# Optimization experiments

Measured on AMD Instinct MI355X. Metric: run time of the kernel, lower is better.

## Reference

```python
import jax, jax.numpy as jnp
import numpy as np
from jax import lax

WINS = [3, 5, 7, 11, 15, 19]
MAXW = 19
PAD = MAXW // 2 + 1          # 10, matches F.pad(..., max_wh//2+1)
NEG_HALF = (-MAXW) // 2      # -10, matches torch's `-self.max_wh // 2` (floor div)
EPS_IN = 1e-5
EPS_DEV = 1e-6


def _conv(x, w, b, dil):
    # x: [B,C,H,W], w: [O,I,kh,kw], 'same' padding with dilation
    y = lax.conv_general_dilated(x, w, (1, 1), 'SAME',
                                 rhs_dilation=(dil, dil),
                                 dimension_numbers=('NCHW', 'OIHW', 'NCHW'))
    return y + b[None, :, None, None]


def _inorm_relu(y):
    # InstanceNorm2d(affine=False): per-sample per-channel over H,W, biased var
    m = jnp.mean(y, axis=(2, 3), keepdims=True)
    v = jnp.mean((y - m) ** 2, axis=(2, 3), keepdims=True)
    return jax.nn.relu((y - m) * lax.rsqrt(v + EPS_IN))


def _integral(x):
    # x: [B,H,W,C] -> padded double cumsum (integral image) [B,H+2P,W+2P,C]
    xp = jnp.pad(x, ((0, 0), (PAD, PAD), (PAD, PAD), (0, 0)))
    return jnp.cumsum(jnp.cumsum(xp, axis=1), axis=2)


def _box_sum(ii, h, w):
    # 4-corner integral-image lookup; slices reproduce torch offsets exactly
    top = MAXW // 2 - h // 2
    bot = top + h
    left = MAXW // 2 - w // 2
    right = left + w
    top0 = NEG_HALF - h // 2 - 1
    bot0 = top0 + h
    left0 = NEG_HALF - w // 2 - 1
    right0 = left0 + w
    return (ii[:, top:top0, left:left0] + ii[:, bot:bot0, right:right0]
            - ii[:, top:top0, right:right0] - ii[:, bot:bot0, left:left0])


def _multi_window_mean(x):
    # x: [B,H,W,1] -> [B,n_wins,H,W,1] of window means
    ii = _integral(x)
    cnt_ii = _integral(jnp.ones_like(x[:1]))  # [1,...] pixel-count integral
    means = [_box_sum(ii, hw, hw) / _box_sum(cnt_ii, hw, hw) for hw in WINS]
    return jnp.stack(means, axis=1)


def _sauvola(x1, k, R):
    E_x = _multi_window_mean(x1)
    E_x2 = _multi_window_mean(x1 * x1)
    dev = jnp.sqrt(jnp.maximum(E_x2 - E_x ** 2, EPS_DEV))
    return E_x * (1.0 + k * (dev / R - 1.0))  # [B,n,H,W,1]


def setup_inputs() -> dict:
    key = jax.random.key(0)
    ks = jax.random.split(key, 16)
    B, H, W = 4, 768, 768
    base = 4
    chans = [1, 4, 8, 12, 16, 20, 24]
    d = {'x': jax.random.uniform(ks[0], (B, 1, H, W), dtype=jnp.float32)}
    names = ['conv1', 'convs1', 'convs2', 'convs3', 'convs4', 'convs5']
    for i, nm in enumerate(names):
        cin, cout = chans[i], chans[i + 1]
        d[nm + '_w'] = jax.random.normal(ks[1 + i], (cout, cin, 3, 3), dtype=jnp.float32) * 0.1
        d[nm + '_b'] = jax.random.normal(ks[7 + i], (cout,), dtype=jnp.float32) * 0.01
    d['conv2_w'] = jax.random.normal(ks[13], (len(WINS), 24, 3, 3), dtype=jnp.float32) * 0.1
    d['conv2_b'] = jax.random.normal(ks[14], (len(WINS),), dtype=jnp.float32) * 0.01
    d['k'] = jnp.full((1, len(WINS), 1, 1, 1), 0.2, dtype=jnp.float32)
    d['R'] = jnp.full((1, len(WINS), 1, 1, 1), 0.5, dtype=jnp.float32)
    d['alpha'] = jnp.full((1, 1, 1, 1), 16.0, dtype=jnp.float32)
    return d


def reference(x, conv1_w, conv1_b, convs1_w, convs1_b, convs2_w, convs2_b,
              convs3_w, convs3_b, convs4_w, convs4_b, convs5_w, convs5_b,
              conv2_w, conv2_b, k, R, alpha):
    y = _inorm_relu(_conv(x, conv1_w, conv1_b, 1))
    for w, b in ((convs1_w, convs1_b), (convs2_w, convs2_b), (convs3_w, convs3_b),
                 (convs4_w, convs4_b), (convs5_w, convs5_b)):
        y = _inorm_relu(_conv(y, w, b, 2))
    f = jax.nn.softmax(_conv(y, conv2_w, conv2_b, 1), axis=1)  # [B,n,H,W]
    x1 = jnp.transpose(x, (0, 2, 3, 1))                        # [B,H,W,1]
    th = _sauvola(x1, k, R)                                    # [B,n,H,W,1]
    th1 = jnp.sum(f[..., None] * th, axis=1)                   # [B,H,W,1]
    diff = (x1 - th1) * alpha / (1.0 - 0.0)                    # img_range (0,1)
    return jnp.transpose(diff, (0, 3, 1, 2))                   # [B,1,H,W]
```

## Files before the change

kernel.cpp:

```cpp
#include <hip/hip_runtime.h>
#include <math.h>

#define BDIM 256
#define BDIM2 512
typedef __bf16 bf16;
typedef __bf16 bf16x4 __attribute__((ext_vector_type(4)));
typedef __bf16 bf16x8 __attribute__((ext_vector_type(8)));
typedef float f32x4 __attribute__((ext_vector_type(4)));
typedef float f32x2 __attribute__((ext_vector_type(2)));

template <bool V> struct BC { static constexpr bool value = V; };

constexpr int B_ = 4, H_ = 768, W_ = 768;
constexpr int HW_ = H_ * W_;
constexpr int TS = 16;
constexpr int NTB = W_ / TS;
constexpr int NBLK = HW_ / (TS * TS);
constexpr int TSR = 16, TSC = 32;
constexpr int NTBC = W_ / TSC;
constexpr int NBLKH = (H_ / TSR) * NTBC;

constexpr int PMAX_FLOATS = 4 * NBLK * 48;
constexpr int OUT_ELEMS   = B_ * HW_;

__device__ void repack_one(const float* __restrict__ src, bf16* __restrict__ dst,
                           int CIN, int CINP, int COUT, int NT16, int KPP)
{
    const int n_ = NT16 * KPP;
    for (int idx = threadIdx.x; idx < n_; idx += BDIM) {
        const int n = idx / KPP, k = idx - n * KPP;
        const int tap = k / CINP, ci = k - tap * CINP;
        float v = 0.f;
        if (n < COUT && tap < 9 && ci < CIN)
            v = src[(n * CIN + ci) * 9 + tap];
        dst[idx] = (bf16)v;
    }
}

__global__ __launch_bounds__(BDIM) void repack_all(
    const float* w0, const float* w1, const float* w2, const float* w3,
    const float* w4, const float* w5, const float* wf,
    bf16* r0, bf16* r1, bf16* r2, bf16* r3, bf16* r4, bf16* r5, bf16* rf)
{
    switch (blockIdx.x) {
        case 0: repack_one(w0, r0, 1,  8,  4,  16, 104); break;
        case 1: repack_one(w1, r1, 4,  8,  8,  16, 104); break;
        case 2: repack_one(w2, r2, 8,  8,  12, 16, 104); break;
        case 3: repack_one(w3, r3, 12, 16, 16, 16, 168); break;
        case 4: repack_one(w4, r4, 16, 16, 20, 32, 168); break;
        case 5: repack_one(w5, r5, 20, 24, 24, 32, 232); break;
        case 6: repack_one(wf, rf, 24, 24, 6,  16, 232); break;
    }
}

template <int CIN, int CINP, int COUT, int DIL, bool FIRST>
__global__ __launch_bounds__(BDIM) void conv_mfma(
    const void* __restrict__ inv,
    const float* __restrict__ prevStats,
    const bf16* __restrict__ wp,
    const float* __restrict__ bias,
    bf16* __restrict__ y,
    float* __restrict__ partials,
    int NBT)
{
    constexpr int TW = TS + 2 * DIL;
    constexpr int KP = ((9 * CINP + 31) / 32) * 32;
    constexpr int KPP = KP + 8;
    constexpr int NT = (COUT + 15) / 16;
    constexpr int KS = KP / 32;
    constexpr int CSTR = (CINP == 16) ? 24 : CINP;
    __shared__ __align__(16) bf16 tile[TW * TW * CSTR];
    __shared__ float sred[4][2 * COUT];

    const int s = blockIdx.x / NBLK;
    const int blk = blockIdx.x - s * NBLK;
    const int ti = blk / NTB, tj = blk - ti * NTB;
    const int i0 = ti * TS - DIL, j0 = tj * TS - DIL;
    const int t = threadIdx.x;
    const bool interior = (i0 >= 0) & (j0 >= 0) &
                          (i0 + TW <= H_) & (j0 + TW <= W_);

    const float* ps = prevStats + s * 2 * CIN;
    auto stage = [&](auto bc) {
        constexpr bool IN = decltype(bc)::value;
        for (int loc = t; loc < TW * TW; loc += BDIM) {
            const int rr = loc / TW, cc = loc - rr * TW;
            const int gi = i0 + rr, gj = j0 + cc;
            bool ok = true;
            if constexpr (!IN)
                ok = (gi >= 0) & (gi < H_) & (gj >= 0) & (gj < W_);
            float lv[CSTR];
#pragma unroll
            for (int c = 0; c < CSTR; ++c) lv[c] = 0.f;
            if (ok) {
                if constexpr (FIRST) {
                    const float* xg = (const float*)inv + (size_t)s * HW_;
                    lv[0] = xg[(size_t)gi * W_ + gj];
                } else {
                    const bf16* ing = (const bf16*)inv +
                                      ((size_t)s * HW_ + (size_t)gi * W_ + gj) * CIN;
                    if constexpr (CIN % 8 == 0) {
#pragma unroll
                        for (int qq = 0; qq < CIN / 8; ++qq) {
                            bf16x8 raw = ((const bf16x8*)ing)[qq];
#pragma unroll
                            for (int u = 0; u < 8; ++u) {
                                const int ci = 8 * qq + u;
                                lv[ci] = fmaxf(fmaf((float)raw[u], ps[2 * ci], ps[2 * ci + 1]), 0.f);
                            }
                        }
                    } else {
#pragma unroll
                        for (int qq = 0; qq < CIN / 4; ++qq) {
                            bf16x4 raw = ((const bf16x4*)ing)[qq];
#pragma unroll
                            for (int u = 0; u < 4; ++u) {
                                const int ci = 4 * qq + u;
                                lv[ci] = fmaxf(fmaf((float)raw[u], ps[2 * ci], ps[2 * ci + 1]), 0.f);
                            }
                        }
                    }
                }
            }
            bf16* lp = tile + loc * CSTR;
#pragma unroll
            for (int g = 0; g < CSTR / 8; ++g) {
                bf16x8 pk;
#pragma unroll
                for (int u = 0; u < 8; ++u) pk[u] = (bf16)lv[8 * g + u];
                *(bf16x8*)(lp + 8 * g) = pk;
            }
        }
    };
    if (interior) stage(BC<true>{}); else stage(BC<false>{});
    __syncthreads();

    const int wave = t >> 6, lane = t & 63, q = lane >> 4, ln = lane & 15;
    f32x4 acc[4][NT];
#pragma unroll
    for (int mt = 0; mt < 4; ++mt)
#pragma unroll
        for (int u = 0; u < NT; ++u) acc[mt][u] = (f32x4){0.f, 0.f, 0.f, 0.f};

    auto aOff = [&](int ks) -> int {
        int k0 = ks * 32 + q * 8;
        int tap = k0 / CINP;
        int ci0 = k0 - tap * CINP;
        if (tap > 8) { tap = 0; ci0 = 0; }
        const int ky = tap / 3, kx = tap - 3 * ky;
        return (ky * DIL * TW + kx * DIL) * CSTR + ci0;
    };

    bf16x8 bfr[NT], bfrN[NT];
    bf16x8 af[4], afN[4];
#pragma unroll
    for (int u = 0; u < NT; ++u)
        bfr[u] = *(const bf16x8*)&wp[(u * 16 + ln) * KPP + q * 8];
    {
        const int ao = aOff(0);
#pragma unroll
        for (int mt = 0; mt < 4; ++mt)
            af[mt] = *(const bf16x8*)&tile[((wave * 4 + mt) * TW + ln) * CSTR + ao];
    }

#pragma unroll
    for (int ks = 0; ks < KS; ++ks) {
        if (ks + 1 < KS) {
#pragma unroll
            for (int u = 0; u < NT; ++u)
                bfrN[u] = *(const bf16x8*)&wp[(u * 16 + ln) * KPP + (ks + 1) * 32 + q * 8];
            const int ao = aOff(ks + 1);
#pragma unroll
            for (int mt = 0; mt < 4; ++mt)
                afN[mt] = *(const bf16x8*)&tile[((wave * 4 + mt) * TW + ln) * CSTR + ao];
        }
#pragma unroll
        for (int mt = 0; mt < 4; ++mt)
#pragma unroll
            for (int u = 0; u < NT; ++u)
                acc[mt][u] = __builtin_amdgcn_mfma_f32_16x16x32_bf16(
                    af[mt], bfr[u], acc[mt][u], 0, 0, 0);
#pragma unroll
        for (int u = 0; u < NT; ++u) bfr[u] = bfrN[u];
#pragma unroll
        for (int mt = 0; mt < 4; ++mt) af[mt] = afN[mt];
    }

#pragma unroll
    for (int u = 0; u < NT; ++u) {
        const int n = u * 16 + ln;
        const float bv = (n < COUT) ? bias[n] : 0.f;
        float s1 = 0.f, s2 = 0.f;
#pragma unroll
        for (int mt = 0; mt < 4; ++mt)
#pragma unroll
            for (int r = 0; r < 4; ++r) {
                const float v = acc[mt][u][r] + bv;
                acc[mt][u][r] = v;
                s1 += v; s2 += v * v;
            }
        s1 += __shfl_xor(s1, 16); s1 += __shfl_xor(s1, 32);
        s2 += __shfl_xor(s2, 16); s2 += __shfl_xor(s2, 32);
        if (lane < 16 && n < COUT) { sred[wave][n] = s1; sred[wave][COUT + n] = s2; }
    }
    __syncthreads();
    if (t < 2 * COUT) {
        partials[(size_t)t * NBT + (size_t)s * NBLK + blk] =
            sred[0][t] + sred[1][t] + sred[2][t] + sred[3][t];
    }

    bf16* ost = tile;
#pragma unroll
    for (int u = 0; u < NT; ++u) {
        const int n = u * 16 + ln;
        if (n < COUT) {
#pragma unroll
            for (int mt = 0; mt < 4; ++mt)
#pragma unroll
                for (int r = 0; r < 4; ++r) {
                    const int pl = (wave * 4 + mt) * 16 + q * 4 + r;
                    ost[pl * COUT + n] = (bf16)acc[mt][u][r];
                }
        }
    }
    __syncthreads();

    const int lr = t >> 4, lc = t & 15;
    bf16* yp = y + (size_t)s * HW_ * COUT +
               ((size_t)(ti * TS + lr) * W_ + (tj * TS + lc)) * COUT;
    const bf16* sp = ost + t * COUT;
    if constexpr (COUT % 8 == 0) {
#pragma unroll
        for (int g = 0; g < COUT / 8; ++g)
            ((bf16x8*)yp)[g] = ((const bf16x8*)sp)[g];
    } else {
#pragma unroll
        for (int g = 0; g < COUT / 4; ++g)
            ((bf16x4*)yp)[g] = ((const bf16x4*)sp)[g];
    }
}

template <int COUT>
__global__ __launch_bounds__(BDIM) void reduce_stats(
    const float* __restrict__ partials, float* __restrict__ stats, int NBT)
{
    const int s = blockIdx.x / COUT;
    const int co = blockIdx.x - s * COUT;
    const float* P1 = partials + (size_t)co * NBT + (size_t)s * NBLK;
    const float* P2 = partials + (size_t)(COUT + co) * NBT + (size_t)s * NBLK;
    float s1 = 0.f, s2 = 0.f;
    for (int k = threadIdx.x; k < NBLK; k += BDIM) {
        s1 += P1[k];
        s2 += P2[k];
    }
#pragma unroll
    for (int off = 32; off; off >>= 1) {
        s1 += __shfl_xor(s1, off);
        s2 += __shfl_xor(s2, off);
    }
    __shared__ float l1[4], l2[4];
    const int lane = threadIdx.x & 63, wave = threadIdx.x >> 6;
    if (lane == 0) { l1[wave] = s1; l2[wave] = s2; }
    __syncthreads();
    if (threadIdx.x == 0) {
        float t1 = l1[0] + l1[1] + l1[2] + l1[3];
        float t2 = l2[0] + l2[1] + l2[2] + l2[3];
        float m = t1 / (float)HW_;
        float var = t2 / (float)HW_ - m * m;
        const float rs = rsqrtf(var + 1e-5f);
        stats[((size_t)s * COUT + co) * 2 + 0] = rs;
        stats[((size_t)s * COUT + co) * 2 + 1] = -m * rs;
    }
}

__global__ __launch_bounds__(BDIM2) void conv2_sauvola(
    const bf16* __restrict__ in, const float* __restrict__ prevStats,
    const bf16* __restrict__ wp, const float* __restrict__ bias,
    const float* __restrict__ x,
    const float* __restrict__ kArr, const float* __restrict__ RArr,
    const float* __restrict__ alphaP, float* __restrict__ outp)
{
    constexpr int CIN = 24, CINP = 24, COUT = 6;
    constexpr int TWR = TSR + 2;
    constexpr int TWC = TSC + 2;
    constexpr int KPP = 232, KS = 7, CSTR = 24;
    constexpr int R9 = 9;
    constexpr int HR = TSR + 2 * R9;
    constexpr int HC = TSC + 2 * R9;
    constexpr int IST = 51;
    constexpr int SLOG_STR = 7;
    __shared__ __align__(16) bf16 tile[TWR * TWC * CSTR];
    __shared__ __align__(16) f32x2 I12[(HR + 1) * IST];

    const int s = blockIdx.x / NBLKH;
    const int blk = blockIdx.x - s * NBLKH;
    const int ti = blk / NTBC, tj = blk - ti * NTBC;
    const int i0 = ti * TSR - 1, j0 = tj * TSC - 1;
    const int is0 = ti * TSR - R9, js0 = tj * TSC - R9;
    const int t = threadIdx.x;
    const float* xs = x + (size_t)s * HW_;
    const bool interior = (is0 >= 0) & (js0 >= 0) &
                          (is0 + HR <= H_) & (js0 + HC <= W_);

    const float* ps = prevStats + s * 2 * CIN;
    auto stage = [&](auto bc) {
        constexpr bool IN = decltype(bc)::value;
        for (int loc = t; loc < TWR * TWC; loc += BDIM2) {
            const int rr = loc / TWC, cc = loc - rr * TWC;
            const int gi = i0 + rr, gj = j0 + cc;
            bool ok = true;
            if constexpr (!IN)
                ok = (gi >= 0) & (gi < H_) & (gj >= 0) & (gj < W_);
            float lv[CSTR];
#pragma unroll
            for (int c = 0; c < CSTR; ++c) lv[c] = 0.f;
            if (ok) {
                const bf16* ing = in + ((size_t)s * HW_ + (size_t)gi * W_ + gj) * CIN;
#pragma unroll
                for (int qq = 0; qq < CIN / 8; ++qq) {
                    bf16x8 raw = ((const bf16x8*)ing)[qq];
#pragma unroll
                    for (int u = 0; u < 8; ++u) {
                        const int ci = 8 * qq + u;
                        lv[ci] = fmaxf(fmaf((float)raw[u], ps[2 * ci], ps[2 * ci + 1]), 0.f);
                    }
                }
            }
            bf16* lp = tile + loc * CSTR;
#pragma unroll
            for (int g = 0; g < CSTR / 8; ++g) {
                bf16x8 pk;
#pragma unroll
                for (int u = 0; u < 8; ++u) pk[u] = (bf16)lv[8 * g + u];
                *(bf16x8*)(lp + 8 * g) = pk;
            }
        }
        for (int loc = t; loc < HR * HC; loc += BDIM2) {
            const int rr = loc / HC, cc = loc - rr * HC;
            const int gi = is0 + rr, gj = js0 + cc;
            float v;
            if constexpr (IN) {
                v = xs[(size_t)gi * W_ + gj];
            } else {
                v = 0.f;
                if ((gi >= 0) & (gi < H_) & (gj >= 0) & (gj < W_))
                    v = xs[(size_t)gi * W_ + gj];
            }
            I12[(rr + 1) * IST + cc + 1] = (f32x2){v, v * v};
        }
    };
    if (interior) stage(BC<true>{}); else stage(BC<false>{});
    for (int idx = t; idx < IST + HR; idx += BDIM2) {
        if (idx < IST) I12[idx] = (f32x2){0.f, 0.f};
        else I12[(idx - IST + 1) * IST] = (f32x2){0.f, 0.f};
    }
    __syncthreads();

    const int wave = t >> 6, lane = t & 63, q = lane >> 4, ln = lane & 15;
    f32x4 acc[4];
#pragma unroll
    for (int mt = 0; mt < 4; ++mt) acc[mt] = (f32x4){0.f, 0.f, 0.f, 0.f};

    auto aOff = [&](int ks) -> int {
        int k0 = ks * 32 + q * 8;
        int tap = k0 / CINP;
        int ci0 = k0 - tap * CINP;
        if (tap > 8) { tap = 0; ci0 = 0; }
        const int ky = tap / 3, kx = tap - 3 * ky;
        return (ky * TWC + kx) * CSTR + ci0;
    };

#pragma unroll
    for (int ks = 0; ks < KS; ++ks) {
        const bf16x8 bfr = *(const bf16x8*)&wp[ln * KPP + ks * 32 + q * 8];
        const int ao = aOff(ks);
#pragma unroll
        for (int mt = 0; mt < 4; ++mt) {
            const int Mt = wave * 4 + mt;
            const bf16x8 af = *(const bf16x8*)
                &tile[(((Mt >> 1)) * TWC + (Mt & 1) * 16 + ln) * CSTR + ao];
            acc[mt] = __builtin_amdgcn_mfma_f32_16x16x32_bf16(af, bfr, acc[mt], 0, 0, 0);
        }
    }
    __syncthreads();

    float* slog = (float*)tile;
    const float bv = (ln < COUT) ? bias[ln] : 0.f;
#pragma unroll
    for (int mt = 0; mt < 4; ++mt)
#pragma unroll
        for (int r = 0; r < 4; ++r)
            if (ln < COUT) {
                const int pl = (wave * 4 + mt) * 16 + q * 4 + r;
                slog[pl * SLOG_STR + ln] = acc[mt][r] + bv;
            }
    if (t < HR) {
        f32x2* row = I12 + (t + 1) * IST;
        f32x2 a = (f32x2){0.f, 0.f};
#pragma unroll 2
        for (int c = 1; c <= HC; ++c) { a += row[c]; row[c] = a; }
    }
    __syncthreads();

    if (t < HC) {
        const int c = t + 1;
        f32x2 a = (f32x2){0.f, 0.f};
#pragma unroll 2
        for (int r = 1; r <= HR; ++r) {
            f32x2* p = &I12[r * IST + c];
            a += *p; *p = a;
        }
    }
    float e0[COUT];
    {
        float mx = slog[t * SLOG_STR];
#pragma unroll
        for (int co = 1; co < COUT; ++co) mx = fmaxf(mx, slog[t * SLOG_STR + co]);
        float sm = 0.f;
#pragma unroll
        for (int co = 0; co < COUT; ++co) { e0[co] = __expf(slog[t * SLOG_STR + co] - mx); sm += e0[co]; }
        const float inv = 1.f / sm;
#pragma unroll
        for (int co = 0; co < COUT; ++co) e0[co] *= inv;
    }
    float c0w[6], c1w[6];
#pragma unroll
    for (int wi = 0; wi < 6; ++wi) {
        const float kk = kArr[wi], rr = RArr[wi];
        c0w[wi] = kk / rr;
        c1w[wi] = 1.f - kk;
    }
    const int pr0 = t >> 5, pc0 = t & 31;
    const int gi0 = ti * TSR + pr0, gj0 = tj * TSC + pc0;
    const float xv0 = xs[(size_t)gi0 * W_ + gj0];
    const float alpha = alphaP[0];
    __syncthreads();

    const int wins[6] = {3, 5, 7, 11, 15, 19};
    const float invc_tab[6] = {1.f / 9.f,  1.f / 25.f,  1.f / 49.f,
                               1.f / 121.f, 1.f / 225.f, 1.f / 361.f};
    float th1 = 0.f;
    if (interior) {
#pragma unroll
        for (int wi = 0; wi < 6; ++wi) {
            const int r = wins[wi] >> 1;
            const float invc = invc_tab[wi];
            const int top = pr0 + R9 - r, bot = pr0 + R9 + r + 1;
            const int lef = pc0 + R9 - r, rig = pc0 + R9 + r + 1;
            const f32x2 Atl = I12[top * IST + lef];
            const f32x2 Atr = I12[top * IST + rig];
            const f32x2 Abl = I12[bot * IST + lef];
            const f32x2 Abr = I12[bot * IST + rig];
            const f32x2 sm2 = Abr - Atr - Abl + Atl;
            const float Ex = sm2.x * invc;
            const float Ex2 = sm2.y * invc;
            const float dev = sqrtf(fmaxf(Ex2 - Ex * Ex, 1e-6f));
            const float th = Ex * fmaf(dev, c0w[wi], c1w[wi]);
            th1 = fmaf(e0[wi], th, th1);
        }
    } else {
#pragma unroll
        for (int wi = 0; wi < 6; ++wi) {
            const int r = wins[wi] >> 1;
            const int r0 = max(gi0 - r, 0), r1i = min(gi0 + r, H_ - 1);
            const int c0 = max(gj0 - r, 0), c1 = min(gj0 + r, W_ - 1);
            const float invc = 1.f / (float)((r1i - r0 + 1) * (c1 - c0 + 1));
            const int top = pr0 + R9 - r, bot = pr0 + R9 + r + 1;
            const int lef = pc0 + R9 - r, rig = pc0 + R9 + r + 1;
            const f32x2 Atl = I12[top * IST + lef];
            const f32x2 Atr = I12[top * IST + rig];
            const f32x2 Abl = I12[bot * IST + lef];
            const f32x2 Abr = I12[bot * IST + rig];
            const f32x2 sm2 = Abr - Atr - Abl + Atl;
            const float Ex = sm2.x * invc;
            const float Ex2 = sm2.y * invc;
            const float dev = sqrtf(fmaxf(Ex2 - Ex * Ex, 1e-6f));
            const float th = Ex * fmaf(dev, c0w[wi], c1w[wi]);
            th1 = fmaf(e0[wi], th, th1);
        }
    }
    outp[(size_t)s * HW_ + (size_t)gi0 * W_ + gj0] = (xv0 - th1) * alpha;
}

extern "C" void kernel_launch(void* const* d_in, const int* in_sizes, int n_in,
                              void* d_out, int out_size, void* d_ws, size_t ws_size,
                              hipStream_t stream) {
    const float* x   = (const float*)d_in[0];
    const float* w0  = (const float*)d_in[1];  const float* b0 = (const float*)d_in[2];
    const float* w1  = (const float*)d_in[3];  const float* b1 = (const float*)d_in[4];
    const float* w2  = (const float*)d_in[5];  const float* b2 = (const float*)d_in[6];
    const float* w3  = (const float*)d_in[7];  const float* b3 = (const float*)d_in[8];
    const float* w4  = (const float*)d_in[9];  const float* b4 = (const float*)d_in[10];
    const float* w5  = (const float*)d_in[11]; const float* b5 = (const float*)d_in[12];
    const float* wf  = (const float*)d_in[13]; const float* bf = (const float*)d_in[14];
    const float* kA  = (const float*)d_in[15];
    const float* RA  = (const float*)d_in[16];
    const float* alp = (const float*)d_in[17];
    float* out = (float*)d_out;
    (void)n_in; (void)in_sizes; (void)out_size;

    float* partials = out + (OUT_ELEMS - PMAX_FLOATS - 256);
    float* stats    = out + (OUT_ELEMS - 224);

    auto need = [](int nb) -> size_t {
        size_t o = 0;
        auto al = [&](size_t bytes) { o += (bytes + 255) & ~(size_t)255; };
        al((size_t)nb * HW_ * 20 * 2);
        al((size_t)nb * HW_ * 24 * 2);
        al(1664 * 2); al(1664 * 2); al(1664 * 2); al(2688 * 2);
        al(5376 * 2); al(7424 * 2); al(3712 * 2);
        return o;
    };
    int nb = 1;
    if (ws_size >= need(4)) nb = 4;
    else if (ws_size >= need(2)) nb = 2;

    char* ws = (char*)d_ws;
    size_t off = 0;
    auto alloc = [&](size_t bytes) -> void* {
        void* p = ws + off;
        off += (bytes + 255) & ~(size_t)255;
        return p;
    };
    bf16*  bufA = (bf16*)alloc((size_t)nb * HW_ * 20 * 2);
    bf16*  bufB = (bf16*)alloc((size_t)nb * HW_ * 24 * 2);
    bf16* r0 = (bf16*)alloc(1664 * 2);
    bf16* r1 = (bf16*)alloc(1664 * 2);
    bf16* r2 = (bf16*)alloc(1664 * 2);
    bf16* r3 = (bf16*)alloc(2688 * 2);
    bf16* r4 = (bf16*)alloc(5376 * 2);
    bf16* r5 = (bf16*)alloc(7424 * 2);
    bf16* rf = (bf16*)alloc(3712 * 2);

    const dim3 blk(BDIM);
    const int cgc = nb * NBLK;
    const int cgh = nb * NBLKH;
    const int NBT = nb * NBLK;

    repack_all<<<7, blk, 0, stream>>>(w0, w1, w2, w3, w4, w5, wf,
                                      r0, r1, r2, r3, r4, r5, rf);

    for (int it = 0; it < B_ / nb; ++it) {
        const float* xc   = x   + (size_t)it * nb * HW_;
        float*       outc = out + (size_t)it * nb * HW_;

        conv_mfma<1, 8, 4, 1, true><<<cgc, blk, 0, stream>>>(xc, nullptr, r0, b0, bufA, partials, NBT);
        reduce_stats<4><<<nb * 4, blk, 0, stream>>>(partials, stats, NBT);

        conv_mfma<4, 8, 8, 2, false><<<cgc, blk, 0, stream>>>(bufA, stats, r1, b1, bufB, partials, NBT);
        reduce_stats<8><<<nb * 8, blk, 0, stream>>>(partials, stats, NBT);

        conv_mfma<8, 8, 12, 2, false><<<cgc, blk, 0, stream>>>(bufB, stats, r2, b2, bufA, partials, NBT);
        reduce_stats<12><<<nb * 12, blk, 0, stream>>>(partials, stats, NBT);

        conv_mfma<12, 16, 16, 2, false><<<cgc, blk, 0, stream>>>(bufA, stats, r3, b3, bufB, partials, NBT);
        reduce_stats<16><<<nb * 16, blk, 0, stream>>>(partials, stats, NBT);

        conv_mfma<16, 16, 20, 2, false><<<cgc, blk, 0, stream>>>(bufB, stats, r4, b4, bufA, partials, NBT);
        reduce_stats<20><<<nb * 20, blk, 0, stream>>>(partials, stats, NBT);

        conv_mfma<20, 24, 24, 2, false><<<cgc, blk, 0, stream>>>(bufA, stats, r5, b5, bufB, partials, NBT);
        reduce_stats<24><<<nb * 24, blk, 0, stream>>>(partials, stats, NBT);

        conv2_sauvola<<<cgh, dim3(BDIM2), 0, stream>>>(
            bufB, stats, rf, bf, xc, kA, RA, alp, outc);
    }
}
```

Measured before the change: 411.0 us.

## Swizzle blocks across XCDs, parallelize integral scan, use fast rcp/sqrt

Remaps block indices so consecutive tiles land on the same XCD, which is meant to improve L2 locality of halo reads. The serial row and column prefix scans of the integral image are split into two halves processed by more threads, followed by fix-up passes that add the first half's carry into the second. Division and sqrt are replaced by hardware approximate rcp/sqrt builtins. The added barriers and fix-up passes cost extra work, and the approximate math slightly changes numerics.

```diff
diff --git a/kernel.cpp b/kernel.cpp
--- a/kernel.cpp
+++ b/kernel.cpp
@@ -22,6 +22,11 @@
 
 constexpr int PMAX_FLOATS = 4 * NBLK * 48;
 constexpr int OUT_ELEMS   = B_ * HW_;
+
+__device__ inline int xcd_swz(int b, int n) {
+    const int q = n >> 3;
+    return (b & 7) * q + (b >> 3);
+}
 
 __device__ void repack_one(const float* __restrict__ src, bf16* __restrict__ dst,
                            int CIN, int CINP, int COUT, int NT16, int KPP)
@@ -72,8 +77,9 @@
     __shared__ __align__(16) bf16 tile[TW * TW * CSTR];
     __shared__ float sred[4][2 * COUT];
 
-    const int s = blockIdx.x / NBLK;
-    const int blk = blockIdx.x - s * NBLK;
+    const int bid = xcd_swz(blockIdx.x, gridDim.x);
+    const int s = bid / NBLK;
+    const int blk = bid - s * NBLK;
     const int ti = blk / NTB, tj = blk - ti * NTB;
     const int i0 = ti * TS - DIL, j0 = tj * TS - DIL;
     const int t = threadIdx.x;
@@ -292,8 +298,9 @@
     __shared__ __align__(16) bf16 tile[TWR * TWC * CSTR];
     __shared__ __align__(16) f32x2 I12[(HR + 1) * IST];
 
-    const int s = blockIdx.x / NBLKH;
-    const int blk = blockIdx.x - s * NBLKH;
+    const int bid = xcd_swz(blockIdx.x, gridDim.x);
+    const int s = bid / NBLKH;
+    const int blk = bid - s * NBLKH;
     const int ti = blk / NTBC, tj = blk - ti * NTBC;
     const int i0 = ti * TSR - 1, j0 = tj * TSC - 1;
     const int is0 = ti * TSR - R9, js0 = tj * TSC - R9;
@@ -394,22 +401,29 @@
                 const int pl = (wave * 4 + mt) * 16 + q * 4 + r;
                 slog[pl * SLOG_STR + ln] = acc[mt][r] + bv;
             }
-    if (t < HR) {
-        f32x2* row = I12 + (t + 1) * IST;
-        f32x2 a = (f32x2){0.f, 0.f};
-#pragma unroll 2
-        for (int c = 1; c <= HC; ++c) { a += row[c]; row[c] = a; }
-    }
-    __syncthreads();
-
-    if (t < HC) {
-        const int c = t + 1;
-        f32x2 a = (f32x2){0.f, 0.f};
-#pragma unroll 2
-        for (int r = 1; r <= HR; ++r) {
-            f32x2* p = &I12[r * IST + c];
-            a += *p; *p = a;
-        }
+    if (t < 68) {
+        const int row = (t < 34 ? t : t - 34) + 1;
+        const int c0 = (t < 34) ? 1 : 26;
+        f32x2* p = I12 + row * IST + c0;
+        f32x2 a = p[0];
+#pragma unroll 5
+        for (int c = 1; c < 25; ++c) { a += p[c]; p[c] = a; }
+    }
+    __syncthreads();
+
+    for (int idx = t; idx < 34 * 25; idx += BDIM2) {
+        const int row = idx / 25 + 1, col = idx % 25 + 26;
+        I12[row * IST + col] += I12[row * IST + 25];
+    }
+    __syncthreads();
+
+    if (t < 100) {
+        const int col = (t < 50 ? t : t - 50) + 1;
+        const int r0 = (t < 50) ? 1 : 18;
+        f32x2* p = I12 + r0 * IST + col;
+        f32x2 a = *p;
+#pragma unroll 4
+        for (int r = 1; r < 17; ++r) { a += p[r * IST]; p[r * IST] = a; }
     }
     float e0[COUT];
     {
@@ -419,7 +433,7 @@
         float sm = 0.f;
 #pragma unroll
         for (int co = 0; co < COUT; ++co) { e0[co] = __expf(slog[t * SLOG_STR + co] - mx); sm += e0[co]; }
-        const float inv = 1.f / sm;
+        const float inv = __builtin_amdgcn_rcpf(sm);
 #pragma unroll
         for (int co = 0; co < COUT; ++co) e0[co] *= inv;
     }
@@ -434,6 +448,12 @@
     const int gi0 = ti * TSR + pr0, gj0 = tj * TSC + pc0;
     const float xv0 = xs[(size_t)gi0 * W_ + gj0];
     const float alpha = alphaP[0];
+    __syncthreads();
+
+    for (int idx = t; idx < 17 * 50; idx += BDIM2) {
+        const int row = idx / 50 + 18, col = idx % 50 + 1;
+        I12[row * IST + col] += I12[17 * IST + col];
+    }
     __syncthreads();
 
     const int wins[6] = {3, 5, 7, 11, 15, 19};
@@ -454,7 +474,7 @@
             const f32x2 sm2 = Abr - Atr - Abl + Atl;
             const float Ex = sm2.x * invc;
             const float Ex2 = sm2.y * invc;
-            const float dev = sqrtf(fmaxf(Ex2 - Ex * Ex, 1e-6f));
+            const float dev = __builtin_amdgcn_sqrtf(fmaxf(Ex2 - Ex * Ex, 1e-6f));
             const float th = Ex * fmaf(dev, c0w[wi], c1w[wi]);
             th1 = fmaf(e0[wi], th, th1);
         }
@@ -464,7 +484,7 @@
             const int r = wins[wi] >> 1;
             const int r0 = max(gi0 - r, 0), r1i = min(gi0 + r, H_ - 1);
             const int c0 = max(gj0 - r, 0), c1 = min(gj0 + r, W_ - 1);
-            const float invc = 1.f / (float)((r1i - r0 + 1) * (c1 - c0 + 1));
+            const float invc = __builtin_amdgcn_rcpf((float)((r1i - r0 + 1) * (c1 - c0 + 1)));
             const int top = pr0 + R9 - r, bot = pr0 + R9 + r + 1;
             const int lef = pc0 + R9 - r, rig = pc0 + R9 + r + 1;
             const f32x2 Atl = I12[top * IST + lef];
@@ -474,7 +494,7 @@
             const f32x2 sm2 = Abr - Atr - Abl + Atl;
             const float Ex = sm2.x * invc;
             const float Ex2 = sm2.y * invc;
-            const float dev = sqrtf(fmaxf(Ex2 - Ex * Ex, 1e-6f));
+            const float dev = __builtin_amdgcn_sqrtf(fmaxf(Ex2 - Ex * Ex, 1e-6f));
             const float th = Ex * fmaf(dev, c0w[wi], c1w[wi]);
             th1 = fmaf(e0[wi], th, th1);
         }
```

New measurement: 380.8 us. 7.4% less time.
